# Kernel optimization log

Hardware: AMD Instinct MI355X
Metric: run time of the kernel (lower is better)

The kernel has to match this reference:

```python
import jax, jax.numpy as jnp
import numpy as np

B, T, I, H, L = 64, 1024, 64, 512, 2


def setup_inputs() -> dict:
    key = jax.random.key(0)
    ks = jax.random.split(key, 4 * L + 4)
    k = 1.0 / np.sqrt(H)
    inp = {"x": jax.random.normal(ks[0], (B, T, I), dtype=jnp.float32)}
    in_sizes = [I] + [H] * (L - 1)
    for l in range(L):
        base = 1 + 4 * l
        inp[f"w_ih{l}"] = jax.random.uniform(ks[base + 0], (3 * H, in_sizes[l]), minval=-k, maxval=k, dtype=jnp.float32)
        inp[f"w_hh{l}"] = jax.random.uniform(ks[base + 1], (3 * H, H), minval=-k, maxval=k, dtype=jnp.float32)
        inp[f"b_ih{l}"] = jax.random.uniform(ks[base + 2], (3 * H,), minval=-k, maxval=k, dtype=jnp.float32)
        inp[f"b_hh{l}"] = jax.random.uniform(ks[base + 3], (3 * H,), minval=-k, maxval=k, dtype=jnp.float32)
    kf = 1.0 / np.sqrt(H)
    inp["fc_w"] = jax.random.uniform(ks[-2], (I, H), minval=-kf, maxval=kf, dtype=jnp.float32)
    inp["fc_b"] = jax.random.uniform(ks[-1], (I,), minval=-kf, maxval=kf, dtype=jnp.float32)
    return inp


def _gru_layer(x, w_ih, w_hh, b_ih, b_hh):
    # x: [B, T, in]; precompute input-side gates as one big GEMM
    xg = jnp.einsum('bti,gi->btg', x, w_ih) + b_ih  # [B, T, 3H]
    h0 = jnp.zeros((x.shape[0], w_hh.shape[1]), x.dtype)

    def step(h, xg_t):
        hg = h @ w_hh.T + b_hh                     # [B, 3H]
        xr, xz, xn = jnp.split(xg_t, 3, axis=-1)
        hr, hz, hn = jnp.split(hg, 3, axis=-1)
        r = jax.nn.sigmoid(xr + hr)
        z = jax.nn.sigmoid(xz + hz)
        n = jnp.tanh(xn + r * hn)
        h_new = (1.0 - z) * n + z * h
        return h_new, h_new

    _, ys = jax.lax.scan(step, h0, jnp.swapaxes(xg, 0, 1))  # ys: [T, B, H]
    return jnp.swapaxes(ys, 0, 1)


def reference(x, w_ih0, w_hh0, b_ih0, b_hh0, w_ih1, w_hh1, b_ih1, b_hh1, fc_w, fc_b):
    h = _gru_layer(x, w_ih0, w_hh0, b_ih0, b_hh0)
    h = _gru_layer(h, w_ih1, w_hh1, b_ih1, b_hh1)
    return h @ fc_w.T + fc_b
```

## Files before the change

kernel.cpp:

```cpp
#include <hip/hip_runtime.h>
#include <hip/hip_bf16.h>

#define T_TOTAL 1024
#define BATCH   64
#define HID     512

__device__ __forceinline__ float fast_sigmoid(float x) {
    return 1.f / (1.f + __expf(-x));
}
__device__ __forceinline__ float fast_tanh(float x) {
    float ax = fabsf(x);
    float e  = __expf(-2.f * ax);
    float t  = (1.f - e) / (1.f + e);
    return copysignf(t, x);
}

template<int BM, int BN, int TM, int TN>
__global__ __launch_bounds__(256, 2)
void gemm_bt_k(const float* __restrict__ A, const float* __restrict__ W,
               const float* __restrict__ bias, float* __restrict__ C,
               int K, int T, int Tc, int t0, int N)
{
    constexpr int BK = 16;
    constexpr int WSTR = BN + (BN / 32) * 4;
    static_assert(BM / TM == 16 && BN / TN == 16, "256 threads required");
    __shared__ float As[BK][BM + 4];
    __shared__ float Ws[BK][WSTR];

    const int tid = threadIdx.x;
    const int tx  = tid & 15;
    const int ty  = tid >> 4;
    const int m0  = blockIdx.y * BM;
    const int n0  = blockIdx.x * BN;
    const int nA  = tx * TN;
    const int nsw = nA + ((nA >> 5) << 2);

    float acc[TM][TN];
#pragma unroll
    for (int i = 0; i < TM; ++i)
#pragma unroll
        for (int j = 0; j < TN; ++j) acc[i][j] = 0.f;

    for (int k0 = 0; k0 < K; k0 += BK) {
#pragma unroll
        for (int i = 0; i < (BM * BK) / 1024; ++i) {
            int id = tid + (i << 8);
            int m  = id >> 2;
            int kq = (id & 3) << 2;
            int mloc = m0 + m;
            int rowg = (mloc / Tc) * T + t0 + (mloc % Tc);
            const float4 v = *reinterpret_cast<const float4*>(A + (size_t)rowg * K + k0 + kq);
            As[kq + 0][m] = v.x; As[kq + 1][m] = v.y;
            As[kq + 2][m] = v.z; As[kq + 3][m] = v.w;
        }
#pragma unroll
        for (int i = 0; i < (BN * BK) / 1024; ++i) {
            int id = tid + (i << 8);
            int n  = id >> 2;
            int kq = (id & 3) << 2;
            const float4 v = *reinterpret_cast<const float4*>(W + (size_t)(n0 + n) * K + k0 + kq);
            int np = n + ((n >> 5) << 2);
            Ws[kq + 0][np] = v.x; Ws[kq + 1][np] = v.y;
            Ws[kq + 2][np] = v.z; Ws[kq + 3][np] = v.w;
        }
        __syncthreads();
#pragma unroll
        for (int k = 0; k < BK; ++k) {
            float a[TM], b[TN];
#pragma unroll
            for (int i = 0; i < TM; i += 4)
                *reinterpret_cast<float4*>(&a[i]) =
                    *reinterpret_cast<const float4*>(&As[k][ty * TM + i]);
#pragma unroll
            for (int j = 0; j < TN; j += 4)
                *reinterpret_cast<float4*>(&b[j]) =
                    *reinterpret_cast<const float4*>(&Ws[k][nsw + j]);
#pragma unroll
            for (int i = 0; i < TM; ++i)
#pragma unroll
                for (int j = 0; j < TN; ++j)
                    acc[i][j] = fmaf(a[i], b[j], acc[i][j]);
        }
        __syncthreads();
    }
#pragma unroll
    for (int i = 0; i < TM; ++i) {
        const size_t crow = (size_t)(m0 + ty * TM + i) * N + n0 + nA;
#pragma unroll
        for (int j = 0; j < TN; j += 4) {
            float4 bv = *reinterpret_cast<const float4*>(bias + n0 + nA + j);
            float4 v;
            v.x = acc[i][j + 0] + bv.x; v.y = acc[i][j + 1] + bv.y;
            v.z = acc[i][j + 2] + bv.z; v.w = acc[i][j + 3] + bv.w;
            *reinterpret_cast<float4*>(C + crow + j) = v;
        }
    }
}

__global__ __launch_bounds__(512, 2)
void gru_scan(const float* __restrict__ xg,
              const float* __restrict__ w_hh,
              const float* __restrict__ b_hh,
              float* __restrict__ y,
              unsigned long long* __restrict__ hbuf,
              int t0, int Tc, int tagbase)
{
    const int tid = threadIdx.x;
    const int grp = blockIdx.x & 31;
    const int os  = blockIdx.x >> 5;
    const int D0  = os << 6;
    const int d   = tid & 63;
    const int kc  = tid >> 6;
    const int bg  = grp << 1;

    __shared__ float h_lds[2][1024];
    __shared__ float part[2][8 * 392];

    float4 w4[3][16];
#pragma unroll
    for (int g = 0; g < 3; ++g) {
        const float* wr = w_hh + (size_t)(g * 512 + D0 + d) * 512 + kc * 64;
#pragma unroll
        for (int j = 0; j < 16; ++j)
            w4[g][j] = *reinterpret_cast<const float4*>(wr + (j << 2));
    }
    float bias_r = 0.f, bias_z = 0.f, bias_n = 0.f;
    if (tid < 128) {
        bias_r = b_hh[       D0 + d];
        bias_z = b_hh[ 512 + D0 + d];
        bias_n = b_hh[1024 + D0 + d];
    }
    const int b_loc = tid >> 6;

    for (int tl = 0; tl < Tc; ++tl) {
        const int tg = t0 + tl;
        float* hl = h_lds[tl & 1];
        float* pt = part[tl & 1];

        float xr = 0.f, xz = 0.f, xn = 0.f;
        if (tid < 128) {
            const size_t rowo = ((size_t)(bg + b_loc) * Tc + tl) * 1536 + D0 + d;
            xr = xg[rowo];
            xz = xg[rowo + 512];
            xn = xg[rowo + 1024];
        }

        if (tg == 0) {
            hl[      kc * 64 + d] = 0.f;
            hl[512 + kc * 64 + d] = 0.f;
        } else {
            const unsigned long long* hsrc =
                hbuf + (size_t)(grp * 2 + ((tg - 1) & 1)) * 1024 + kc * 64;
            const unsigned int tagexp = (unsigned int)(tagbase + tl - 1);
            unsigned long long v0 = 0, v1 = 0;
            unsigned int pend = 0x3u;
            while (pend) {
                if (pend & 1u)
                    v0 = __hip_atomic_load(hsrc + d,
                            __ATOMIC_RELAXED, __HIP_MEMORY_SCOPE_AGENT);
                if (pend & 2u)
                    v1 = __hip_atomic_load(hsrc + 512 + d,
                            __ATOMIC_RELAXED, __HIP_MEMORY_SCOPE_AGENT);
                if ((pend & 1u) && (unsigned int)(v0 >> 32) == tagexp) {
                    union { unsigned int u; float f; } cv; cv.u = (unsigned int)v0;
                    hl[kc * 64 + d] = cv.f;
                    pend &= ~1u;
                }
                if ((pend & 2u) && (unsigned int)(v1 >> 32) == tagexp) {
                    union { unsigned int u; float f; } cv; cv.u = (unsigned int)v1;
                    hl[512 + kc * 64 + d] = cv.f;
                    pend &= ~2u;
                }
                if (pend) __builtin_amdgcn_s_sleep(1);
            }
        }
        __builtin_amdgcn_s_waitcnt(0xC07F);

        float acc[3][2];
#pragma unroll
        for (int g = 0; g < 3; ++g) { acc[g][0] = 0.f; acc[g][1] = 0.f; }
        const float* hb = hl + kc * 64;
#pragma unroll
        for (int j = 0; j < 16; ++j) {
            const float4 h0 = *reinterpret_cast<const float4*>(hb + (j << 2));
            const float4 h1 = *reinterpret_cast<const float4*>(hb + 512 + (j << 2));
#pragma unroll
            for (int g = 0; g < 3; ++g) {
                const float4 wv = w4[g][j];
                acc[g][0] = fmaf(wv.x, h0.x, acc[g][0]);
                acc[g][0] = fmaf(wv.y, h0.y, acc[g][0]);
                acc[g][0] = fmaf(wv.z, h0.z, acc[g][0]);
                acc[g][0] = fmaf(wv.w, h0.w, acc[g][0]);
                acc[g][1] = fmaf(wv.x, h1.x, acc[g][1]);
                acc[g][1] = fmaf(wv.y, h1.y, acc[g][1]);
                acc[g][1] = fmaf(wv.z, h1.z, acc[g][1]);
                acc[g][1] = fmaf(wv.w, h1.w, acc[g][1]);
            }
        }
        {
            float* pp = pt + kc * 392 + d;
#pragma unroll
            for (int g = 0; g < 3; ++g) {
                pp[g * 128]      = acc[g][0];
                pp[g * 128 + 64] = acc[g][1];
            }
        }
        __syncthreads();

        if (tid < 128) {
            float sr = bias_r, sz = bias_z, sn = bias_n;
#pragma unroll
            for (int q = 0; q < 8; ++q) {
                sr += pt[q * 392 +       tid];
                sz += pt[q * 392 + 128 + tid];
                sn += pt[q * 392 + 256 + tid];
            }
            const int D = D0 + d;
            const float hp = hl[b_loc * 512 + D];
            const float r  = fast_sigmoid(xr + sr);
            const float z  = fast_sigmoid(xz + sz);
            const float nv = fast_tanh(xn + r * sn);
            const float h  = (1.f - z) * nv + z * hp;
            union { float f; unsigned int u; } cv; cv.f = h;
            const unsigned long long pk =
                ((unsigned long long)(unsigned int)(tagbase + tl) << 32) | cv.u;
            unsigned long long* hdst =
                hbuf + (size_t)(grp * 2 + (tg & 1)) * 1024 + b_loc * 512 + D;
            __hip_atomic_store(hdst, pk, __ATOMIC_RELAXED,
                               __HIP_MEMORY_SCOPE_AGENT);
            y[((size_t)(bg + b_loc) * T_TOTAL + tg) * HID + D] = h;
        }
    }
}

extern "C" void kernel_launch(void* const* d_in, const int* in_sizes, int n_in,
                              void* d_out, int out_size, void* d_ws, size_t ws_size,
                              hipStream_t stream)
{
    const float* x       = (const float*)d_in[0];
    const float* w_ih[2] = {(const float*)d_in[1], (const float*)d_in[5]};
    const float* w_hh[2] = {(const float*)d_in[2], (const float*)d_in[6]};
    const float* b_ih[2] = {(const float*)d_in[3], (const float*)d_in[7]};
    const float* b_hh[2] = {(const float*)d_in[4], (const float*)d_in[8]};
    const float* fc_w    = (const float*)d_in[9];
    const float* fc_b    = (const float*)d_in[10];
    float* out = (float*)d_out;

    const size_t Y_BYTES = (size_t)BATCH * T_TOTAL * HID * 4;
    const size_t H_BYTES = (size_t)32 * 2 * 2 * 512 * 8;
    int Tc = 256;
    while (Tc > 32) {
        size_t need = (size_t)BATCH * Tc * 1536 * 4 + Y_BYTES + H_BYTES;
        if (need <= ws_size) break;
        Tc >>= 1;
    }

    char* p = (char*)d_ws;
    float* xg_buf = (float*)p;                 p += (size_t)BATCH * Tc * 1536 * 4;
    float* y_buf  = (float*)p;                 p += Y_BYTES;
    unsigned long long* hbuf = (unsigned long long*)p;

    const int nchunks = T_TOTAL / Tc;
    for (int L = 0; L < 2; ++L) {
        const float* A = L ? y_buf : x;
        const int K    = L ? HID : 64;
        for (int c = 0; c < nchunks; ++c) {
            dim3 g1(1536 / 128, (BATCH * Tc) / 128);
            gemm_bt_k<128, 128, 8, 8><<<g1, 256, 0, stream>>>(
                A, w_ih[L], b_ih[L], xg_buf, K, T_TOTAL, Tc, c * Tc, 1536);
            gru_scan<<<256, 512, 0, stream>>>(
                xg_buf, w_hh[L], b_hh[L], y_buf, hbuf,
                c * Tc, Tc, (L << 11) + c * Tc);
        }
    }
    dim3 g2(64 / 64, (BATCH * T_TOTAL) / 128);
    gemm_bt_k<128, 64, 8, 4><<<g2, 256, 0, stream>>>(
        y_buf, fc_w, fc_b, out, HID, BATCH * T_TOTAL, BATCH * T_TOTAL, 0, 64);
}
```

Measured before the change: 6.391 ms.

## Overlap next chunk's input-gate GEMM with current GRU scan in fused kernel

Merges the recurrent scan kernel and the input-projection GEMM into one launch. The first 256 blocks run the scan for the current chunk at raised priority, while the extra blocks compute the input gates for the next chunk (or next layer's first chunk) into a second, double-buffered xg buffer. The goal is to hide the GEMM behind the latency-bound scan and cut the number of serialized launches. The costs are doubled workspace for xg, a shared-memory union sized for both roles, and the risk that co-scheduled GEMM blocks slow the spin-waiting scan blocks or interfere with their co-residency.

```diff
diff --git a/kernel.cpp b/kernel.cpp
--- a/kernel.cpp
+++ b/kernel.cpp
@@ -4,6 +4,7 @@
 #define T_TOTAL 1024
 #define BATCH   64
 #define HID     512
+#define NSCAN   256
 
 __device__ __forceinline__ float fast_sigmoid(float x) {
     return 1.f / (1.f + __expf(-x));
@@ -97,138 +98,220 @@
     }
 }
 
+struct ScanSmem {
+    float h_lds[2][1024];
+    float part[2][8 * 392];
+};
+struct GemmSmem {
+    float As[16][132];
+    float Ws[16][144];
+};
+union FusedSmem { ScanSmem s; GemmSmem g; };
+
 __global__ __launch_bounds__(512, 2)
-void gru_scan(const float* __restrict__ xg,
-              const float* __restrict__ w_hh,
-              const float* __restrict__ b_hh,
-              float* __restrict__ y,
-              unsigned long long* __restrict__ hbuf,
-              int t0, int Tc, int tagbase)
+void scan_gemm_fused(const float* __restrict__ xg,
+                     const float* __restrict__ w_hh,
+                     const float* __restrict__ b_hh,
+                     float* __restrict__ y,
+                     unsigned long long* __restrict__ hbuf,
+                     int t0, int Tc, int tagbase,
+                     const float* __restrict__ gA,
+                     const float* __restrict__ gW,
+                     const float* __restrict__ gbias,
+                     float* __restrict__ gC,
+                     int gK, int gt0, int gNB)
 {
+    __shared__ FusedSmem sm;
     const int tid = threadIdx.x;
-    const int grp = blockIdx.x & 31;
-    const int os  = blockIdx.x >> 5;
-    const int D0  = os << 6;
-    const int d   = tid & 63;
-    const int kc  = tid >> 6;
-    const int bg  = grp << 1;
-
-    __shared__ float h_lds[2][1024];
-    __shared__ float part[2][8 * 392];
-
-    float4 w4[3][16];
-#pragma unroll
-    for (int g = 0; g < 3; ++g) {
-        const float* wr = w_hh + (size_t)(g * 512 + D0 + d) * 512 + kc * 64;
-#pragma unroll
-        for (int j = 0; j < 16; ++j)
-            w4[g][j] = *reinterpret_cast<const float4*>(wr + (j << 2));
-    }
-    float bias_r = 0.f, bias_z = 0.f, bias_n = 0.f;
-    if (tid < 128) {
-        bias_r = b_hh[       D0 + d];
-        bias_z = b_hh[ 512 + D0 + d];
-        bias_n = b_hh[1024 + D0 + d];
-    }
-    const int b_loc = tid >> 6;
-
-    for (int tl = 0; tl < Tc; ++tl) {
-        const int tg = t0 + tl;
-        float* hl = h_lds[tl & 1];
-        float* pt = part[tl & 1];
-
-        float xr = 0.f, xz = 0.f, xn = 0.f;
+
+    if (blockIdx.x < NSCAN) {
+        __builtin_amdgcn_s_setprio(2);
+        const int grp = blockIdx.x & 31;
+        const int os  = blockIdx.x >> 5;
+        const int D0  = os << 6;
+        const int d   = tid & 63;
+        const int kc  = tid >> 6;
+        const int bg  = grp << 1;
+
+        float4 w4[3][16];
+#pragma unroll
+        for (int g = 0; g < 3; ++g) {
+            const float* wr = w_hh + (size_t)(g * 512 + D0 + d) * 512 + kc * 64;
+#pragma unroll
+            for (int j = 0; j < 16; ++j)
+                w4[g][j] = *reinterpret_cast<const float4*>(wr + (j << 2));
+        }
+        float bias_r = 0.f, bias_z = 0.f, bias_n = 0.f;
         if (tid < 128) {
-            const size_t rowo = ((size_t)(bg + b_loc) * Tc + tl) * 1536 + D0 + d;
-            xr = xg[rowo];
-            xz = xg[rowo + 512];
-            xn = xg[rowo + 1024];
-        }
-
-        if (tg == 0) {
-            hl[      kc * 64 + d] = 0.f;
-            hl[512 + kc * 64 + d] = 0.f;
-        } else {
-            const unsigned long long* hsrc =
-                hbuf + (size_t)(grp * 2 + ((tg - 1) & 1)) * 1024 + kc * 64;
-            const unsigned int tagexp = (unsigned int)(tagbase + tl - 1);
-            unsigned long long v0 = 0, v1 = 0;
-            unsigned int pend = 0x3u;
-            while (pend) {
-                if (pend & 1u)
-                    v0 = __hip_atomic_load(hsrc + d,
-                            __ATOMIC_RELAXED, __HIP_MEMORY_SCOPE_AGENT);
-                if (pend & 2u)
-                    v1 = __hip_atomic_load(hsrc + 512 + d,
-                            __ATOMIC_RELAXED, __HIP_MEMORY_SCOPE_AGENT);
-                if ((pend & 1u) && (unsigned int)(v0 >> 32) == tagexp) {
-                    union { unsigned int u; float f; } cv; cv.u = (unsigned int)v0;
-                    hl[kc * 64 + d] = cv.f;
-                    pend &= ~1u;
+            bias_r = b_hh[       D0 + d];
+            bias_z = b_hh[ 512 + D0 + d];
+            bias_n = b_hh[1024 + D0 + d];
+        }
+        const int b_loc = tid >> 6;
+
+        for (int tl = 0; tl < Tc; ++tl) {
+            const int tg = t0 + tl;
+            float* hl = sm.s.h_lds[tl & 1];
+            float* pt = sm.s.part[tl & 1];
+
+            float xr = 0.f, xz = 0.f, xn = 0.f;
+            if (tid < 128) {
+                const size_t rowo = ((size_t)(bg + b_loc) * Tc + tl) * 1536 + D0 + d;
+                xr = xg[rowo];
+                xz = xg[rowo + 512];
+                xn = xg[rowo + 1024];
+            }
+
+            if (tg == 0) {
+                hl[      kc * 64 + d] = 0.f;
+                hl[512 + kc * 64 + d] = 0.f;
+            } else {
+                const unsigned long long* hsrc =
+                    hbuf + (size_t)(grp * 2 + ((tg - 1) & 1)) * 1024 + kc * 64;
+                const unsigned int tagexp = (unsigned int)(tagbase + tl - 1);
+                unsigned long long v0 = 0, v1 = 0;
+                unsigned int pend = 0x3u;
+                while (pend) {
+                    if (pend & 1u)
+                        v0 = __hip_atomic_load(hsrc + d,
+                                __ATOMIC_RELAXED, __HIP_MEMORY_SCOPE_AGENT);
+                    if (pend & 2u)
+                        v1 = __hip_atomic_load(hsrc + 512 + d,
+                                __ATOMIC_RELAXED, __HIP_MEMORY_SCOPE_AGENT);
+                    if ((pend & 1u) && (unsigned int)(v0 >> 32) == tagexp) {
+                        union { unsigned int u; float f; } cv; cv.u = (unsigned int)v0;
+                        hl[kc * 64 + d] = cv.f;
+                        pend &= ~1u;
+                    }
+                    if ((pend & 2u) && (unsigned int)(v1 >> 32) == tagexp) {
+                        union { unsigned int u; float f; } cv; cv.u = (unsigned int)v1;
+                        hl[512 + kc * 64 + d] = cv.f;
+                        pend &= ~2u;
+                    }
+                    if (pend) __builtin_amdgcn_s_sleep(1);
                 }
-                if ((pend & 2u) && (unsigned int)(v1 >> 32) == tagexp) {
-                    union { unsigned int u; float f; } cv; cv.u = (unsigned int)v1;
-                    hl[512 + kc * 64 + d] = cv.f;
-                    pend &= ~2u;
+            }
+            __builtin_amdgcn_s_waitcnt(0xC07F);
+
+            float acc[3][2];
+#pragma unroll
+            for (int g = 0; g < 3; ++g) { acc[g][0] = 0.f; acc[g][1] = 0.f; }
+            const float* hb = hl + kc * 64;
+#pragma unroll
+            for (int j = 0; j < 16; ++j) {
+                const float4 h0 = *reinterpret_cast<const float4*>(hb + (j << 2));
+                const float4 h1 = *reinterpret_cast<const float4*>(hb + 512 + (j << 2));
+#pragma unroll
+                for (int g = 0; g < 3; ++g) {
+                    const float4 wv = w4[g][j];
+                    acc[g][0] = fmaf(wv.x, h0.x, acc[g][0]);
+                    acc[g][0] = fmaf(wv.y, h0.y, acc[g][0]);
+                    acc[g][0] = fmaf(wv.z, h0.z, acc[g][0]);
+                    acc[g][0] = fmaf(wv.w, h0.w, acc[g][0]);
+                    acc[g][1] = fmaf(wv.x, h1.x, acc[g][1]);
+                    acc[g][1] = fmaf(wv.y, h1.y, acc[g][1]);
+                    acc[g][1] = fmaf(wv.z, h1.z, acc[g][1]);
+                    acc[g][1] = fmaf(wv.w, h1.w, acc[g][1]);
                 }
-                if (pend) __builtin_amdgcn_s_sleep(1);
-            }
-        }
-        __builtin_amdgcn_s_waitcnt(0xC07F);
-
-        float acc[3][2];
-#pragma unroll
-        for (int g = 0; g < 3; ++g) { acc[g][0] = 0.f; acc[g][1] = 0.f; }
-        const float* hb = hl + kc * 64;
-#pragma unroll
-        for (int j = 0; j < 16; ++j) {
-            const float4 h0 = *reinterpret_cast<const float4*>(hb + (j << 2));
-            const float4 h1 = *reinterpret_cast<const float4*>(hb + 512 + (j << 2));
-#pragma unroll
-            for (int g = 0; g < 3; ++g) {
-                const float4 wv = w4[g][j];
-                acc[g][0] = fmaf(wv.x, h0.x, acc[g][0]);
-                acc[g][0] = fmaf(wv.y, h0.y, acc[g][0]);
-                acc[g][0] = fmaf(wv.z, h0.z, acc[g][0]);
-                acc[g][0] = fmaf(wv.w, h0.w, acc[g][0]);
-                acc[g][1] = fmaf(wv.x, h1.x, acc[g][1]);
-                acc[g][1] = fmaf(wv.y, h1.y, acc[g][1]);
-                acc[g][1] = fmaf(wv.z, h1.z, acc[g][1]);
-                acc[g][1] = fmaf(wv.w, h1.w, acc[g][1]);
-            }
-        }
-        {
-            float* pp = pt + kc * 392 + d;
-#pragma unroll
-            for (int g = 0; g < 3; ++g) {
-                pp[g * 128]      = acc[g][0];
-                pp[g * 128 + 64] = acc[g][1];
-            }
-        }
-        __syncthreads();
-
-        if (tid < 128) {
-            float sr = bias_r, sz = bias_z, sn = bias_n;
-#pragma unroll
-            for (int q = 0; q < 8; ++q) {
-                sr += pt[q * 392 +       tid];
-                sz += pt[q * 392 + 128 + tid];
-                sn += pt[q * 392 + 256 + tid];
-            }
-            const int D = D0 + d;
-            const float hp = hl[b_loc * 512 + D];
-            const float r  = fast_sigmoid(xr + sr);
-            const float z  = fast_sigmoid(xz + sz);
-            const float nv = fast_tanh(xn + r * sn);
-            const float h  = (1.f - z) * nv + z * hp;
-            union { float f; unsigned int u; } cv; cv.f = h;
-            const unsigned long long pk =
-                ((unsigned long long)(unsigned int)(tagbase + tl) << 32) | cv.u;
-            unsigned long long* hdst =
-                hbuf + (size_t)(grp * 2 + (tg & 1)) * 1024 + b_loc * 512 + D;
-            __hip_atomic_store(hdst, pk, __ATOMIC_RELAXED,
-                               __HIP_MEMORY_SCOPE_AGENT);
-            y[((size_t)(bg + b_loc) * T_TOTAL + tg) * HID + D] = h;
+            }
+            {
+                float* pp = pt + kc * 392 + d;
+#pragma unroll
+                for (int g = 0; g < 3; ++g) {
+                    pp[g * 128]      = acc[g][0];
+                    pp[g * 128 + 64] = acc[g][1];
+                }
+            }
+            __syncthreads();
+
+            if (tid < 128) {
+                float sr = bias_r, sz = bias_z, sn = bias_n;
+#pragma unroll
+                for (int q = 0; q < 8; ++q) {
+                    sr += pt[q * 392 +       tid];
+                    sz += pt[q * 392 + 128 + tid];
+                    sn += pt[q * 392 + 256 + tid];
+                }
+                const int D = D0 + d;
+                const float hp = hl[b_loc * 512 + D];
+                const float r  = fast_sigmoid(xr + sr);
+                const float z  = fast_sigmoid(xz + sz);
+                const float nv = fast_tanh(xn + r * sn);
+                const float h  = (1.f - z) * nv + z * hp;
+                union { float f; unsigned int u; } cv; cv.f = h;
+                const unsigned long long pk =
+                    ((unsigned long long)(unsigned int)(tagbase + tl) << 32) | cv.u;
+                unsigned long long* hdst =
+                    hbuf + (size_t)(grp * 2 + (tg & 1)) * 1024 + b_loc * 512 + D;
+                __hip_atomic_store(hdst, pk, __ATOMIC_RELAXED,
+                                   __HIP_MEMORY_SCOPE_AGENT);
+                y[((size_t)(bg + b_loc) * T_TOTAL + tg) * HID + D] = h;
+            }
+        }
+    } else {
+        const int bid = blockIdx.x - NSCAN;
+        if (bid >= gNB) return;
+        const int NXT = 12;
+        const int by  = bid / NXT;
+        const int bx  = bid - by * NXT;
+        const int m0  = by << 7;
+        const int n0  = bx << 7;
+        const int tx  = tid & 31;
+        const int ty  = tid >> 5;
+        const int nA  = tx << 2;
+        const int nsw = nA + ((nA >> 5) << 2);
+
+        const int mA   = tid >> 2;
+        const int kqA  = (tid & 3) << 2;
+        const int mloc = m0 + mA;
+        const int rowg = (mloc / Tc) * T_TOTAL + gt0 + (mloc % Tc);
+
+        float acc[8][4];
+#pragma unroll
+        for (int i = 0; i < 8; ++i)
+#pragma unroll
+            for (int j = 0; j < 4; ++j) acc[i][j] = 0.f;
+
+        for (int k0 = 0; k0 < gK; k0 += 16) {
+            {
+                const float4 v = *reinterpret_cast<const float4*>(
+                    gA + (size_t)rowg * gK + k0 + kqA);
+                sm.g.As[kqA + 0][mA] = v.x; sm.g.As[kqA + 1][mA] = v.y;
+                sm.g.As[kqA + 2][mA] = v.z; sm.g.As[kqA + 3][mA] = v.w;
+            }
+            {
+                const float4 v = *reinterpret_cast<const float4*>(
+                    gW + (size_t)(n0 + mA) * gK + k0 + kqA);
+                int np = mA + ((mA >> 5) << 2);
+                sm.g.Ws[kqA + 0][np] = v.x; sm.g.Ws[kqA + 1][np] = v.y;
+                sm.g.Ws[kqA + 2][np] = v.z; sm.g.Ws[kqA + 3][np] = v.w;
+            }
+            __syncthreads();
+#pragma unroll
+            for (int k = 0; k < 16; ++k) {
+                float a[8], b[4];
+                *reinterpret_cast<float4*>(&a[0]) =
+                    *reinterpret_cast<const float4*>(&sm.g.As[k][ty * 8]);
+                *reinterpret_cast<float4*>(&a[4]) =
+                    *reinterpret_cast<const float4*>(&sm.g.As[k][ty * 8 + 4]);
+                *reinterpret_cast<float4*>(&b[0]) =
+                    *reinterpret_cast<const float4*>(&sm.g.Ws[k][nsw]);
+#pragma unroll
+                for (int i = 0; i < 8; ++i)
+#pragma unroll
+                    for (int j = 0; j < 4; ++j)
+                        acc[i][j] = fmaf(a[i], b[j], acc[i][j]);
+            }
+            __syncthreads();
+        }
+        const float4 bv = *reinterpret_cast<const float4*>(gbias + n0 + nA);
+#pragma unroll
+        for (int i = 0; i < 8; ++i) {
+            float4 v;
+            v.x = acc[i][0] + bv.x; v.y = acc[i][1] + bv.y;
+            v.z = acc[i][2] + bv.z; v.w = acc[i][3] + bv.w;
+            *reinterpret_cast<float4*>(
+                gC + (size_t)(m0 + ty * 8 + i) * 1536 + n0 + nA) = v;
         }
     }
 }
@@ -250,30 +333,46 @@
     const size_t H_BYTES = (size_t)32 * 2 * 2 * 512 * 8;
     int Tc = 256;
     while (Tc > 32) {
-        size_t need = (size_t)BATCH * Tc * 1536 * 4 + Y_BYTES + H_BYTES;
+        size_t need = 2 * ((size_t)BATCH * Tc * 1536 * 4) + Y_BYTES + H_BYTES;
         if (need <= ws_size) break;
         Tc >>= 1;
     }
+    const size_t XG_BYTES = (size_t)BATCH * Tc * 1536 * 4;
 
     char* p = (char*)d_ws;
-    float* xg_buf = (float*)p;                 p += (size_t)BATCH * Tc * 1536 * 4;
-    float* y_buf  = (float*)p;                 p += Y_BYTES;
+    float* xgb[2];
+    xgb[0] = (float*)p;                        p += XG_BYTES;
+    xgb[1] = (float*)p;                        p += XG_BYTES;
+    float* y_buf = (float*)p;                  p += Y_BYTES;
     unsigned long long* hbuf = (unsigned long long*)p;
 
-    const int nchunks = T_TOTAL / Tc;
-    for (int L = 0; L < 2; ++L) {
-        const float* A = L ? y_buf : x;
-        const int K    = L ? HID : 64;
-        for (int c = 0; c < nchunks; ++c) {
-            dim3 g1(1536 / 128, (BATCH * Tc) / 128);
-            gemm_bt_k<128, 128, 8, 8><<<g1, 256, 0, stream>>>(
-                A, w_ih[L], b_ih[L], xg_buf, K, T_TOTAL, Tc, c * Tc, 1536);
-            gru_scan<<<256, 512, 0, stream>>>(
-                xg_buf, w_hh[L], b_hh[L], y_buf, hbuf,
-                c * Tc, Tc, (L << 11) + c * Tc);
-        }
-    }
-    dim3 g2(64 / 64, (BATCH * T_TOTAL) / 128);
+    const int nch = T_TOTAL / Tc;
+    const int nsteps = 2 * nch;
+    const int WNB = ((BATCH * Tc) / 128) * 12;
+
+    {
+        dim3 g1(12, (BATCH * Tc) / 128);
+        gemm_bt_k<128, 128, 8, 8><<<g1, 256, 0, stream>>>(
+            x, w_ih[0], b_ih[0], xgb[0], 64, T_TOTAL, Tc, 0, 1536);
+    }
+
+    for (int i = 0; i < nsteps; ++i) {
+        const int L = i / nch, c = i % nch;
+        const bool has_next = (i + 1 < nsteps);
+        const int L2 = (i + 1) / nch, c2 = (i + 1) % nch;
+        const int gNB = has_next ? WNB : 0;
+        dim3 grid(NSCAN + gNB);
+        scan_gemm_fused<<<grid, 512, 0, stream>>>(
+            xgb[i & 1], w_hh[L], b_hh[L], y_buf, hbuf,
+            c * Tc, Tc, (L << 11) + c * Tc,
+            has_next ? (L2 ? y_buf : x) : nullptr,
+            has_next ? w_ih[L2] : nullptr,
+            has_next ? b_ih[L2] : nullptr,
+            has_next ? xgb[(i + 1) & 1] : nullptr,
+            L2 ? 512 : 64, c2 * Tc, gNB);
+    }
+
+    dim3 g2(1, (BATCH * T_TOTAL) / 128);
     gemm_bt_k<128, 64, 8, 4><<<g2, 256, 0, stream>>>(
         y_buf, fc_w, fc_b, out, HID, BATCH * T_TOTAL, BATCH * T_TOTAL, 0, 64);
 }
```

Result: slower. 8.052 ms (+26.0%).
